# Kernel tuning notes

Hardware: AMD Instinct MI355X
Metric: run time of the kernel (lower is better)

Reference implementation:

```python
import jax, jax.numpy as jnp
import numpy as np

QUERY_DIM = 512
HEADS = 8
DIM_HEAD = 64
INNER = HEADS * DIM_HEAD  # 512


def setup_inputs() -> dict:
    key = jax.random.key(0)
    ks = jax.random.split(key, 7)
    B, N, M = 4, 2048, 2048
    s = 0.02
    return {
        "x": jax.random.normal(ks[0], (B, N, QUERY_DIM), dtype=jnp.float32),
        "context": jax.random.normal(ks[1], (B, M, QUERY_DIM), dtype=jnp.float32),
        "Wq": jax.random.normal(ks[2], (QUERY_DIM, INNER), dtype=jnp.float32) * s,
        "Wk": jax.random.normal(ks[3], (QUERY_DIM, INNER), dtype=jnp.float32) * s,
        "Wv": jax.random.normal(ks[4], (QUERY_DIM, INNER), dtype=jnp.float32) * s,
        "Wo": jax.random.normal(ks[5], (INNER, QUERY_DIM), dtype=jnp.float32) * s,
        "bo": jnp.zeros((QUERY_DIM,), dtype=jnp.float32),
    }


def reference(x, context, Wq, Wk, Wv, Wo, bo):
    B, N, _ = x.shape
    M = context.shape[1]
    # projections, split heads: [B, H, N, D]
    q = (x @ Wq).reshape(B, N, HEADS, DIM_HEAD).transpose(0, 2, 1, 3)
    k = (context @ Wk).reshape(B, M, HEADS, DIM_HEAD).transpose(0, 2, 1, 3)
    v = (context @ Wv).reshape(B, M, HEADS, DIM_HEAD).transpose(0, 2, 1, 3)
    scale = 1.0 / jnp.sqrt(jnp.float32(DIM_HEAD))
    attn = jnp.einsum('bhid,bhjd->bhij', q, k) * scale  # [B,H,N,M]
    attn = jax.nn.softmax(attn, axis=-1)
    out = jnp.einsum('bhij,bhjd->bhid', attn, v)  # [B,H,N,D]
    out = out.transpose(0, 2, 1, 3).reshape(B, N, INNER)
    return out @ Wo + bo
```

## Files before the change

### kernel.cpp

```cpp
#include <hip/hip_runtime.h>


typedef short bf16x8 __attribute__((ext_vector_type(8)));
typedef float f32x4 __attribute__((ext_vector_type(4)));
typedef float f32x16 __attribute__((ext_vector_type(16)));
typedef unsigned int u32x4 __attribute__((ext_vector_type(4)));
typedef unsigned short u16x8 __attribute__((ext_vector_type(8)));

#define NB 4
#define NN 2048
#define QD 512
#define DH 64
#define QSCALE 0.18033688011112042f

__device__ __forceinline__ unsigned short f2bf(float f) {
  unsigned u = __float_as_uint(f);
  unsigned r = (u + 0x7fffu + ((u >> 16) & 1u)) >> 16;
  return (unsigned short)r;
}

__device__ __forceinline__ unsigned cvtpk(float a, float b) {
  unsigned r;
  asm("v_cvt_pk_bf16_f32 %0, %1, %2" : "=v"(r) : "v"(a), "v"(b));
  return r;
}

__device__ __forceinline__ void pl32swap(unsigned& a, unsigned& b) {
  asm("v_permlane32_swap_b32 %0, %1" : "+v"(a), "+v"(b));
}

__device__ __forceinline__ void gload16(const void* g, void* l) {
  __builtin_amdgcn_global_load_lds((const __attribute__((address_space(1))) unsigned int*)g,
                                   (__attribute__((address_space(3))) unsigned int*)l, 16, 0, 0);
}

__global__ __launch_bounds__(256) void cvt_inputs(const float* __restrict__ x,
                                                  const float* __restrict__ ctx,
                                                  unsigned short* __restrict__ xb,
                                                  unsigned short* __restrict__ cb) {
  int i = blockIdx.x * 256 + threadIdx.x;
  const int total = (NB * NN * QD) / 4;
  if (i < total) {
    float4 v = ((const float4*)x)[i];
    ushort4 o;
    o.x = f2bf(v.x); o.y = f2bf(v.y); o.z = f2bf(v.z); o.w = f2bf(v.w);
    ((ushort4*)xb)[i] = o;
    float4 w = ((const float4*)ctx)[i];
    ushort4 p;
    p.x = f2bf(w.x); p.y = f2bf(w.y); p.z = f2bf(w.z); p.w = f2bf(w.w);
    ((ushort4*)cb)[i] = p;
  }
}

__global__ __launch_bounds__(256) void cvt_weights(const float* __restrict__ Wq, const float* __restrict__ Wk,
                                                   const float* __restrict__ Wv, const float* __restrict__ Wo,
                                                   unsigned short* __restrict__ wqt, unsigned short* __restrict__ wkt,
                                                   unsigned short* __restrict__ wvt, unsigned short* __restrict__ wot) {
  __shared__ float t[32][33];
  const float* W = blockIdx.z == 0 ? Wq : blockIdx.z == 1 ? Wk : blockIdx.z == 2 ? Wv : Wo;
  unsigned short* O = blockIdx.z == 0 ? wqt : blockIdx.z == 1 ? wkt : blockIdx.z == 2 ? wvt : wot;
  int c0 = blockIdx.x * 32, k0 = blockIdx.y * 32;
  int tx = threadIdx.x, ty = threadIdx.y;
#pragma unroll
  for (int j = 0; j < 4; j++) t[ty + 8 * j][tx] = W[(k0 + ty + 8 * j) * QD + c0 + tx];
  __syncthreads();
#pragma unroll
  for (int j = 0; j < 4; j++) O[(c0 + ty + 8 * j) * QD + k0 + tx] = f2bf(t[tx][ty + 8 * j]);
}

__global__ __launch_bounds__(256, 2) void qkv_gemm(const unsigned short* __restrict__ xb,
                                                   const unsigned short* __restrict__ cb,
                                                   const unsigned short* __restrict__ wqt,
                                                   const unsigned short* __restrict__ wkt,
                                                   const unsigned short* __restrict__ wvt,
                                                   unsigned short* __restrict__ q_ws,
                                                   unsigned short* __restrict__ k_ws,
                                                   unsigned short* __restrict__ v_ws) {
  __shared__ __align__(16) char sAB[2][32768];
  const int z = blockIdx.z;
  const unsigned short* A = (z == 0) ? xb : cb;
  const unsigned short* Bt = (z == 0) ? wqt : (z == 1) ? wkt : wvt;
  const int lane = threadIdx.x & 63, wid = threadIdx.x >> 6;
  const int lo = lane & 15, hi = lane >> 4;
  const int wm = wid >> 1, wn = wid & 1;
  const int r0 = blockIdx.x * 128, c0 = blockIdx.y * 128;
  const int r8 = lane >> 3, c8l = lane & 7;

#define STAGEQ(K0, BUF)                                                      \
  do {                                                                       \
    char* b_ = sAB[BUF];                                                     \
    _Pragma("unroll") for (int i_ = 0; i_ < 4; ++i_) {                       \
      int chunk_ = wid * 4 + i_;                                             \
      int row_ = chunk_ * 8 + r8;                                            \
      gload16(&A[(r0 + row_) * QD + (K0) + c8l * 8], b_ + chunk_ * 1024);    \
      gload16(&Bt[(c0 + row_) * QD + (K0) + c8l * 8],                        \
              b_ + 16384 + chunk_ * 1024);                                   \
    }                                                                        \
  } while (0)

  f32x4 acc[4][4] = {};
  STAGEQ(0, 0);
  for (int ks = 0; ks < 8; ++ks) {
    asm volatile("s_waitcnt vmcnt(0)" ::: "memory");
    __builtin_amdgcn_s_barrier();
    __builtin_amdgcn_sched_barrier(0);
    if (ks + 1 < 8) STAGEQ((ks + 1) * 64, (ks + 1) & 1);
    const unsigned short* sA = (const unsigned short*)sAB[ks & 1];
    const unsigned short* sB = sA + 8192;
#pragma unroll
    for (int kk = 0; kk < 2; kk++) {
      bf16x8 af[4], bfr[4];
#pragma unroll
      for (int t = 0; t < 4; t++) af[t] = *(const bf16x8*)&sA[(wm * 64 + t * 16 + lo) * 64 + (kk * 4 + hi) * 8];
#pragma unroll
      for (int u = 0; u < 4; u++) bfr[u] = *(const bf16x8*)&sB[(wn * 64 + u * 16 + lo) * 64 + (kk * 4 + hi) * 8];
#pragma unroll
      for (int t = 0; t < 4; t++)
#pragma unroll
        for (int u = 0; u < 4; u++)
          acc[t][u] = __builtin_amdgcn_mfma_f32_16x16x32_bf16(af[t], bfr[u], acc[t][u], 0, 0, 0);
    }
  }
#undef STAGEQ

  if (z == 2) {
    __syncthreads();
    unsigned short* tb = (unsigned short*)sAB;
#pragma unroll
    for (int t = 0; t < 4; t++)
#pragma unroll
      for (int u = 0; u < 4; u++)
#pragma unroll
        for (int ri = 0; ri < 4; ri++) {
          int rloc = wm * 64 + t * 16 + hi * 4 + ri;
          int cloc = wn * 64 + u * 16 + lo;
          tb[cloc * 136 + rloc] = f2bf(acc[t][u][ri]);
        }
    __syncthreads();
    const int b = r0 >> 11, n0 = r0 & 2047;
#pragma unroll
    for (int i = 0; i < 8; i++) {
      int hd = i * 16 + (threadIdx.x >> 4);
      int mcol = (threadIdx.x & 15) * 8;
      u16x8 v = *(const u16x8*)&tb[hd * 136 + mcol];
      int h = (c0 + hd) >> 6, d = (c0 + hd) & 63;
      *(u16x8*)&v_ws[(((b << 3) | h) * DH + d) * NN + n0 + mcol] = v;
    }
  } else {
    const float outscale = (z == 0) ? QSCALE : 1.0f;
    unsigned short* Cq = (z == 0) ? q_ws : k_ws;
#pragma unroll
    for (int t = 0; t < 4; t++)
#pragma unroll
      for (int u = 0; u < 4; u++)
#pragma unroll
        for (int ri = 0; ri < 4; ri++) {
          int r = r0 + wm * 64 + t * 16 + hi * 4 + ri;
          int c = c0 + wn * 64 + u * 16 + lo;
          float v = acc[t][u][ri] * outscale;
          int b = r >> 11, n = r & 2047, h = c >> 6, d = c & 63;
          Cq[(((b << 3) | h) * NN + n) * DH + d] = f2bf(v);
        }
  }
}

__global__ __launch_bounds__(512, 4) void flash_attn(const unsigned short* __restrict__ Q,
                                                     const unsigned short* __restrict__ K,
                                                     const unsigned short* __restrict__ Vt,
                                                     unsigned short* __restrict__ po,
                                                     float* __restrict__ pml) {
  __shared__ __align__(16) char sKV[2][16384];
  const int tid = threadIdx.x;
  const int lane = tid & 63, wid = tid >> 6;
  const int l31 = lane & 31, hi = lane >> 5;
  const int bh = blockIdx.x, half = blockIdx.z;
  const int bhK = bh * NN, bhV = bh * DH;
  const int kv0 = half * (NN / 2);
  const int qrow = blockIdx.y * 256 + wid * 32 + l31;
  po += half * (32 * 2048 * 64);
  pml += half * (32 * 2048);

  bf16x8 qf[4];
#pragma unroll
  for (int ks = 0; ks < 4; ks++)
    qf[ks] = *(const bf16x8*)&Q[(bhK + qrow) * DH + ks * 16 + hi * 8];

  const int row_s = tid >> 3, slot_s = tid & 7;
  const int swz = (slot_s ^ (row_s & 7)) * 8;

#define STAGE(J0, BUF)                                                     \
  do {                                                                     \
    char* b_ = (char*)sKV[BUF];                                            \
    gload16(&K[(bhK + (J0) + row_s) * DH + swz], b_ + wid * 1024);         \
    gload16(&Vt[(bhV + row_s) * NN + (J0) + swz], b_ + 8192 + wid * 1024); \
  } while (0)

  float l = 0.f;
  f32x16 o[2] = {};

  STAGE(kv0, 0);

  for (int it = 0; it < 16; ++it) {
    asm volatile("s_waitcnt vmcnt(0)" ::: "memory");
    __builtin_amdgcn_s_barrier();
    __builtin_amdgcn_sched_barrier(0);
    if (it + 1 < 16) STAGE(kv0 + (it + 1) * 64, (it + 1) & 1);
    const char* buf = (const char*)sKV[it & 1];

    f32x16 st[2] = {};
    __builtin_amdgcn_s_setprio(1);
#pragma unroll
    for (int g = 0; g < 2; g++)
#pragma unroll
      for (int ks = 0; ks < 4; ks++) {
        bf16x8 kf = *(const bf16x8*)(buf + (g * 32 + l31) * 128 + (((ks * 2 + hi) ^ (l31 & 7)) << 4));
        st[g] = __builtin_amdgcn_mfma_f32_32x32x16_bf16(kf, qf[ks], st[g], 0, 0, 0);
      }
    __builtin_amdgcn_s_setprio(0);

#pragma unroll
    for (int g = 0; g < 2; g++)
#pragma unroll
      for (int c = 0; c < 16; c++) st[g][c] = __builtin_amdgcn_exp2f(st[g][c]);
    float s8[8];
#pragma unroll
    for (int c = 0; c < 8; c++) s8[c] = (st[0][c] + st[0][c + 8]) + (st[1][c] + st[1][c + 8]);
#pragma unroll
    for (int w = 4; w >= 1; w >>= 1)
#pragma unroll
      for (int c = 0; c < 4; c++)
        if (c < w) s8[c] += s8[c + w];
    l += s8[0] + __shfl_xor(s8[0], 32);

    bf16x8 pf[2][2];
#pragma unroll
    for (int g = 0; g < 2; g++)
#pragma unroll
      for (int s = 0; s < 2; s++) {
        const int cb = s * 8;
        unsigned a0 = cvtpk(st[g][cb + 0], st[g][cb + 1]);
        unsigned a1 = cvtpk(st[g][cb + 2], st[g][cb + 3]);
        unsigned b0 = cvtpk(st[g][cb + 4], st[g][cb + 5]);
        unsigned b1 = cvtpk(st[g][cb + 6], st[g][cb + 7]);
        pl32swap(a0, b0);
        pl32swap(a1, b1);
        union { unsigned u[4]; bf16x8 v; } pu;
        pu.u[0] = a0; pu.u[1] = a1; pu.u[2] = b0; pu.u[3] = b1;
        pf[g][s] = pu.v;
      }

    __builtin_amdgcn_s_setprio(1);
#pragma unroll
    for (int dt = 0; dt < 2; dt++)
#pragma unroll
      for (int g = 0; g < 2; g++)
#pragma unroll
        for (int s = 0; s < 2; s++) {
          int row = dt * 32 + l31;
          bf16x8 vf = *(const bf16x8*)(buf + 8192 + row * 128 + (((g * 4 + s * 2 + hi) ^ (row & 7)) << 4));
          o[dt] = __builtin_amdgcn_mfma_f32_32x32x16_bf16(vf, pf[g][s], o[dt], 0, 0, 0);
        }
    __builtin_amdgcn_s_setprio(0);
  }
#undef STAGE

  float inv = 1.f / l;
  const int rbase = (bh * 2048 + qrow) * 64;
#pragma unroll
  for (int dt = 0; dt < 2; dt++)
#pragma unroll
    for (int cg = 0; cg < 4; cg++) {
      ushort4 w;
      w.x = f2bf(o[dt][cg * 4 + 0] * inv);
      w.y = f2bf(o[dt][cg * 4 + 1] * inv);
      w.z = f2bf(o[dt][cg * 4 + 2] * inv);
      w.w = f2bf(o[dt][cg * 4 + 3] * inv);
      int d0 = dt * 32 + cg * 8 + hi * 4;
      *(ushort4*)&po[rbase + d0] = w;
    }
  if (hi == 0) pml[bh * 2048 + qrow] = l;
}

__global__ __launch_bounds__(256, 2) void out_gemm(const unsigned short* __restrict__ po,
                                                   const float* __restrict__ pml,
                                                   const unsigned short* __restrict__ Bt,
                                                   float* __restrict__ out,
                                                   const float* __restrict__ bias) {
  __shared__ __align__(16) unsigned short sA[128 * 64];
  __shared__ __align__(16) unsigned short sB[64 * 64];
  const unsigned short* po1 = po + 32 * 2048 * 64;
  const float* pml1 = pml + 32 * 2048;
  const int lane = threadIdx.x & 63, wid = threadIdx.x >> 6;
  const int lo = lane & 15, hi = lane >> 4;
  const int wm = wid >> 1, wn = wid & 1;
  const int r0 = blockIdx.x * 128, c0 = blockIdx.y * 64;
  const int r8 = lane >> 3, c8l = lane & 7;
  f32x4 acc[4][2] = {};
  for (int k0 = 0; k0 < QD; k0 += 64) {
    __syncthreads();
    const int h = k0 >> 6;
#pragma unroll
    for (int i = 0; i < 4; i++) {
      int id = i * 256 + threadIdx.x;
      int row = id >> 3, slot = id & 7;
      int r = r0 + row, b = r >> 11, n = r & 2047;
      int pr = ((b << 3) | h) * NN + n;
      float la = pml[pr], lb = pml1[pr];
      float s = __builtin_amdgcn_rcpf(la + lb);
      float wa = la * s, wb = lb * s;
      u32x4 A0 = *(const u32x4*)&po[pr * 64 + slot * 8];
      u32x4 A1 = *(const u32x4*)&po1[pr * 64 + slot * 8];
      u32x4 res;
#pragma unroll
      for (int j = 0; j < 4; j++) {
        float a_lo = __uint_as_float(A0[j] << 16), a_hi = __uint_as_float(A0[j] & 0xffff0000u);
        float b_lo = __uint_as_float(A1[j] << 16), b_hi = __uint_as_float(A1[j] & 0xffff0000u);
        res[j] = cvtpk(a_lo * wa + b_lo * wb, a_hi * wa + b_hi * wb);
      }
      *(u32x4*)((char*)sA + id * 16) = res;
    }
#pragma unroll
    for (int i = 0; i < 2; i++) {
      int chunk = wid * 2 + i;
      int row = chunk * 8 + r8;
      gload16(&Bt[(c0 + row) * QD + k0 + c8l * 8], (char*)sB + chunk * 1024);
    }
    __syncthreads();
#pragma unroll
    for (int kk = 0; kk < 2; kk++) {
      bf16x8 af[4], bfr[2];
#pragma unroll
      for (int t = 0; t < 4; t++) af[t] = *(const bf16x8*)&sA[(wm * 64 + t * 16 + lo) * 64 + (kk * 4 + hi) * 8];
#pragma unroll
      for (int u = 0; u < 2; u++) bfr[u] = *(const bf16x8*)&sB[(wn * 32 + u * 16 + lo) * 64 + (kk * 4 + hi) * 8];
#pragma unroll
      for (int t = 0; t < 4; t++)
#pragma unroll
        for (int u = 0; u < 2; u++)
          acc[t][u] = __builtin_amdgcn_mfma_f32_16x16x32_bf16(af[t], bfr[u], acc[t][u], 0, 0, 0);
    }
  }
#pragma unroll
  for (int t = 0; t < 4; t++)
#pragma unroll
    for (int u = 0; u < 2; u++)
#pragma unroll
      for (int ri = 0; ri < 4; ri++) {
        int r = r0 + wm * 64 + t * 16 + hi * 4 + ri;
        int c = c0 + wn * 32 + u * 16 + lo;
        out[r * QD + c] = acc[t][u][ri] + bias[c];
      }
}

extern "C" void kernel_launch(void* const* d_in, const int* in_sizes, int n_in,
                              void* d_out, int out_size, void* d_ws, size_t ws_size,
                              hipStream_t stream) {
  const float* x   = (const float*)d_in[0];
  const float* ctx = (const float*)d_in[1];
  const float* Wq  = (const float*)d_in[2];
  const float* Wk  = (const float*)d_in[3];
  const float* Wv  = (const float*)d_in[4];
  const float* Wo  = (const float*)d_in[5];
  const float* bo  = (const float*)d_in[6];
  char* ws = (char*)d_ws;

  unsigned short* xb   = (unsigned short*)(ws);
  unsigned short* cb   = (unsigned short*)(ws + 8388608);
  unsigned short* po   = (unsigned short*)(ws);
  unsigned short* wqt  = (unsigned short*)(ws + 16777216);
  unsigned short* wkt  = (unsigned short*)(ws + 17301504);
  unsigned short* wvt  = (unsigned short*)(ws + 17825792);
  unsigned short* wot  = (unsigned short*)(ws + 18350080);
  unsigned short* q_ws = (unsigned short*)(ws + 18874368);
  unsigned short* k_ws = (unsigned short*)(ws + 27262976);
  unsigned short* v_ws = (unsigned short*)(ws + 35651584);
  float*          pml  = (float*)(ws + 44040192);
  float* out = (float*)d_out;

  cvt_inputs<<<4096, 256, 0, stream>>>(x, ctx, xb, cb);
  cvt_weights<<<dim3(16, 16, 4), dim3(32, 8), 0, stream>>>(Wq, Wk, Wv, Wo, wqt, wkt, wvt, wot);

  qkv_gemm<<<dim3(64, 4, 3), 256, 0, stream>>>(xb, cb, wqt, wkt, wvt, q_ws, k_ws, v_ws);

  flash_attn<<<dim3(32, 8, 2), 512, 0, stream>>>(q_ws, k_ws, v_ws, po, pml);

  out_gemm<<<dim3(64, 8), 256, 0, stream>>>(po, pml, wot, out, bo);
}
```

Baseline: 99.45 us.

## Process two 32-row query tiles per wave in flash attention, halving block threads

Each wave now handles 64 query rows (two 32-row MFMA tiles) instead of 32, so every K/V fragment read from LDS feeds two MFMAs. Blocks drop from 512 to 256 threads while still covering 256 query rows, and each thread stages two K/V chunks. This cuts LDS reads per MFMA and barrier overhead per unit of work, at the cost of roughly double accumulator and score registers per thread and fewer waves available to hide latency.

```diff
diff --git a/kernel.cpp b/kernel.cpp
--- a/kernel.cpp
+++ b/kernel.cpp
@@ -164,7 +164,7 @@
   }
 }
 
-__global__ __launch_bounds__(512, 4) void flash_attn(const unsigned short* __restrict__ Q,
+__global__ __launch_bounds__(256, 2) void flash_attn(const unsigned short* __restrict__ Q,
                                                      const unsigned short* __restrict__ K,
                                                      const unsigned short* __restrict__ Vt,
                                                      unsigned short* __restrict__ po,
@@ -176,27 +176,33 @@
   const int bh = blockIdx.x, half = blockIdx.z;
   const int bhK = bh * NN, bhV = bh * DH;
   const int kv0 = half * (NN / 2);
-  const int qrow = blockIdx.y * 256 + wid * 32 + l31;
+  const int qbase = blockIdx.y * 256 + wid * 64;
   po += half * (32 * 2048 * 64);
   pml += half * (32 * 2048);
 
-  bf16x8 qf[4];
-#pragma unroll
-  for (int ks = 0; ks < 4; ks++)
-    qf[ks] = *(const bf16x8*)&Q[(bhK + qrow) * DH + ks * 16 + hi * 8];
-
-  const int row_s = tid >> 3, slot_s = tid & 7;
-  const int swz = (slot_s ^ (row_s & 7)) * 8;
-
-#define STAGE(J0, BUF)                                                     \
-  do {                                                                     \
-    char* b_ = (char*)sKV[BUF];                                            \
-    gload16(&K[(bhK + (J0) + row_s) * DH + swz], b_ + wid * 1024);         \
-    gload16(&Vt[(bhV + row_s) * NN + (J0) + swz], b_ + 8192 + wid * 1024); \
+  bf16x8 qf[4][2];
+#pragma unroll
+  for (int ks = 0; ks < 4; ks++) {
+    qf[ks][0] = *(const bf16x8*)&Q[(bhK + qbase + l31) * DH + ks * 16 + hi * 8];
+    qf[ks][1] = *(const bf16x8*)&Q[(bhK + qbase + 32 + l31) * DH + ks * 16 + hi * 8];
+  }
+
+  const int sl_s = lane & 7;
+
+#define STAGE(J0, BUF)                                                       \
+  do {                                                                       \
+    char* b_ = (char*)sKV[BUF];                                              \
+    _Pragma("unroll") for (int i_ = 0; i_ < 2; ++i_) {                       \
+      int c_ = wid * 2 + i_;                                                 \
+      int row_ = c_ * 8 + (lane >> 3);                                       \
+      int sw_ = (sl_s ^ (row_ & 7)) * 8;                                     \
+      gload16(&K[(bhK + (J0) + row_) * DH + sw_], b_ + c_ * 1024);           \
+      gload16(&Vt[(bhV + row_) * NN + (J0) + sw_], b_ + 8192 + c_ * 1024);   \
+    }                                                                        \
   } while (0)
 
-  float l = 0.f;
-  f32x16 o[2] = {};
+  float l0 = 0.f, l1 = 0.f;
+  f32x16 o[2][2] = {};
 
   STAGE(kv0, 0);
 
@@ -207,47 +213,58 @@
     if (it + 1 < 16) STAGE(kv0 + (it + 1) * 64, (it + 1) & 1);
     const char* buf = (const char*)sKV[it & 1];
 
-    f32x16 st[2] = {};
+    f32x16 st[2][2] = {};
     __builtin_amdgcn_s_setprio(1);
 #pragma unroll
     for (int g = 0; g < 2; g++)
 #pragma unroll
       for (int ks = 0; ks < 4; ks++) {
         bf16x8 kf = *(const bf16x8*)(buf + (g * 32 + l31) * 128 + (((ks * 2 + hi) ^ (l31 & 7)) << 4));
-        st[g] = __builtin_amdgcn_mfma_f32_32x32x16_bf16(kf, qf[ks], st[g], 0, 0, 0);
+        st[g][0] = __builtin_amdgcn_mfma_f32_32x32x16_bf16(kf, qf[ks][0], st[g][0], 0, 0, 0);
+        st[g][1] = __builtin_amdgcn_mfma_f32_32x32x16_bf16(kf, qf[ks][1], st[g][1], 0, 0, 0);
       }
     __builtin_amdgcn_s_setprio(0);
 
 #pragma unroll
+    for (int qt = 0; qt < 2; qt++)
+#pragma unroll
+      for (int g = 0; g < 2; g++)
+#pragma unroll
+        for (int c = 0; c < 16; c++) st[g][qt][c] = __builtin_amdgcn_exp2f(st[g][qt][c]);
+    {
+      float s8a[8], s8b[8];
+#pragma unroll
+      for (int c = 0; c < 8; c++) {
+        s8a[c] = (st[0][0][c] + st[0][0][c + 8]) + (st[1][0][c] + st[1][0][c + 8]);
+        s8b[c] = (st[0][1][c] + st[0][1][c + 8]) + (st[1][1][c] + st[1][1][c + 8]);
+      }
+#pragma unroll
+      for (int w = 4; w >= 1; w >>= 1)
+#pragma unroll
+        for (int c = 0; c < 4; c++)
+          if (c < w) { s8a[c] += s8a[c + w]; s8b[c] += s8b[c + w]; }
+      l0 += s8a[0] + __shfl_xor(s8a[0], 32);
+      l1 += s8b[0] + __shfl_xor(s8b[0], 32);
+    }
+
+    bf16x8 pf[2][2][2];
+#pragma unroll
     for (int g = 0; g < 2; g++)
 #pragma unroll
-      for (int c = 0; c < 16; c++) st[g][c] = __builtin_amdgcn_exp2f(st[g][c]);
-    float s8[8];
-#pragma unroll
-    for (int c = 0; c < 8; c++) s8[c] = (st[0][c] + st[0][c + 8]) + (st[1][c] + st[1][c + 8]);
-#pragma unroll
-    for (int w = 4; w >= 1; w >>= 1)
-#pragma unroll
-      for (int c = 0; c < 4; c++)
-        if (c < w) s8[c] += s8[c + w];
-    l += s8[0] + __shfl_xor(s8[0], 32);
-
-    bf16x8 pf[2][2];
-#pragma unroll
-    for (int g = 0; g < 2; g++)
-#pragma unroll
-      for (int s = 0; s < 2; s++) {
-        const int cb = s * 8;
-        unsigned a0 = cvtpk(st[g][cb + 0], st[g][cb + 1]);
-        unsigned a1 = cvtpk(st[g][cb + 2], st[g][cb + 3]);
-        unsigned b0 = cvtpk(st[g][cb + 4], st[g][cb + 5]);
-        unsigned b1 = cvtpk(st[g][cb + 6], st[g][cb + 7]);
-        pl32swap(a0, b0);
-        pl32swap(a1, b1);
-        union { unsigned u[4]; bf16x8 v; } pu;
-        pu.u[0] = a0; pu.u[1] = a1; pu.u[2] = b0; pu.u[3] = b1;
-        pf[g][s] = pu.v;
-      }
+      for (int s = 0; s < 2; s++)
+#pragma unroll
+        for (int qt = 0; qt < 2; qt++) {
+          const int cb = s * 8;
+          unsigned a0 = cvtpk(st[g][qt][cb + 0], st[g][qt][cb + 1]);
+          unsigned a1 = cvtpk(st[g][qt][cb + 2], st[g][qt][cb + 3]);
+          unsigned b0 = cvtpk(st[g][qt][cb + 4], st[g][qt][cb + 5]);
+          unsigned b1 = cvtpk(st[g][qt][cb + 6], st[g][qt][cb + 7]);
+          pl32swap(a0, b0);
+          pl32swap(a1, b1);
+          union { unsigned u[4]; bf16x8 v; } pu;
+          pu.u[0] = a0; pu.u[1] = a1; pu.u[2] = b0; pu.u[3] = b1;
+          pf[g][s][qt] = pu.v;
+        }
 
     __builtin_amdgcn_s_setprio(1);
 #pragma unroll
@@ -258,27 +275,33 @@
         for (int s = 0; s < 2; s++) {
           int row = dt * 32 + l31;
           bf16x8 vf = *(const bf16x8*)(buf + 8192 + row * 128 + (((g * 4 + s * 2 + hi) ^ (row & 7)) << 4));
-          o[dt] = __builtin_amdgcn_mfma_f32_32x32x16_bf16(vf, pf[g][s], o[dt], 0, 0, 0);
+          o[dt][0] = __builtin_amdgcn_mfma_f32_32x32x16_bf16(vf, pf[g][s][0], o[dt][0], 0, 0, 0);
+          o[dt][1] = __builtin_amdgcn_mfma_f32_32x32x16_bf16(vf, pf[g][s][1], o[dt][1], 0, 0, 0);
         }
     __builtin_amdgcn_s_setprio(0);
   }
 #undef STAGE
 
-  float inv = 1.f / l;
-  const int rbase = (bh * 2048 + qrow) * 64;
-#pragma unroll
-  for (int dt = 0; dt < 2; dt++)
-#pragma unroll
-    for (int cg = 0; cg < 4; cg++) {
-      ushort4 w;
-      w.x = f2bf(o[dt][cg * 4 + 0] * inv);
-      w.y = f2bf(o[dt][cg * 4 + 1] * inv);
-      w.z = f2bf(o[dt][cg * 4 + 2] * inv);
-      w.w = f2bf(o[dt][cg * 4 + 3] * inv);
-      int d0 = dt * 32 + cg * 8 + hi * 4;
-      *(ushort4*)&po[rbase + d0] = w;
-    }
-  if (hi == 0) pml[bh * 2048 + qrow] = l;
+#pragma unroll
+  for (int qt = 0; qt < 2; qt++) {
+    float l = (qt == 0) ? l0 : l1;
+    float inv = 1.f / l;
+    const int qrow = qbase + qt * 32 + l31;
+    const int rbase = (bh * 2048 + qrow) * 64;
+#pragma unroll
+    for (int dt = 0; dt < 2; dt++)
+#pragma unroll
+      for (int cg = 0; cg < 4; cg++) {
+        ushort4 w;
+        w.x = f2bf(o[dt][qt][cg * 4 + 0] * inv);
+        w.y = f2bf(o[dt][qt][cg * 4 + 1] * inv);
+        w.z = f2bf(o[dt][qt][cg * 4 + 2] * inv);
+        w.w = f2bf(o[dt][qt][cg * 4 + 3] * inv);
+        int d0 = dt * 32 + cg * 8 + hi * 4;
+        *(ushort4*)&po[rbase + d0] = w;
+      }
+    if (hi == 0) pml[bh * 2048 + qrow] = l;
+  }
 }
 
 __global__ __launch_bounds__(256, 2) void out_gemm(const unsigned short* __restrict__ po,
@@ -382,7 +405,7 @@
 
   qkv_gemm<<<dim3(64, 4, 3), 256, 0, stream>>>(xb, cb, wqt, wkt, wvt, q_ws, k_ws, v_ws);
 
-  flash_attn<<<dim3(32, 8, 2), 512, 0, stream>>>(q_ws, k_ws, v_ws, po, pml);
+  flash_attn<<<dim3(32, 8, 2), 256, 0, stream>>>(q_ws, k_ws, v_ws, po, pml);
 
   out_gemm<<<dim3(64, 8), 256, 0, stream>>>(po, pml, wot, out, bo);
 }
```

Result: no change. 99.42 us (-0.0%).
